# Kernel tuning notes

Measured on AMD Instinct MI355X. Metric: run time of the kernel, lower is better.

Reference implementation:

```python
import jax, jax.numpy as jnp
import numpy as np

N_NODES = 100000
N_EDGES = 1600000
IN_FEAT = 128
HIDDEN = 64
N_CLASSES = 16


def setup_inputs() -> dict:
    key = jax.random.key(0)
    ks = jax.random.split(key, 8)
    x = jax.random.normal(ks[0], (N_NODES, IN_FEAT), dtype=jnp.float32)
    edge_index = jax.random.randint(ks[1], (2, N_EDGES), 0, N_NODES, dtype=jnp.int64)
    W1 = jax.random.normal(ks[2], (IN_FEAT, HIDDEN), dtype=jnp.float32) / np.sqrt(IN_FEAT)
    b1 = jnp.zeros((HIDDEN,), dtype=jnp.float32)
    W2 = jax.random.normal(ks[3], (HIDDEN, HIDDEN), dtype=jnp.float32) / np.sqrt(HIDDEN)
    b2 = jnp.zeros((HIDDEN,), dtype=jnp.float32)
    Wl = jax.random.normal(ks[4], (HIDDEN, N_CLASSES), dtype=jnp.float32) / np.sqrt(HIDDEN)
    bl = jnp.zeros((N_CLASSES,), dtype=jnp.float32)
    return {"x": x, "edge_index": edge_index, "W1": W1, "b1": b1,
            "W2": W2, "b2": b2, "Wl": Wl, "bl": bl}


def _gcn_norm(edge_index, n_nodes, dtype):
    # PyG GCNConv default: add self-loops, symmetric normalization
    # A_hat = D^{-1/2} (A + I) D^{-1/2}, degree computed at destination (col).
    loop = jnp.arange(n_nodes, dtype=edge_index.dtype)
    src = jnp.concatenate([edge_index[0], loop])
    dst = jnp.concatenate([edge_index[1], loop])
    deg = jax.ops.segment_sum(jnp.ones_like(dst, dtype=dtype), dst, num_segments=n_nodes)
    dinv = jnp.where(deg > 0, jax.lax.rsqrt(deg), 0.0).astype(dtype)
    norm = dinv[src] * dinv[dst]  # [E + N]
    return src, dst, norm


def _gcn_conv(h, src, dst, norm, W, b, n_nodes):
    hw = h @ W                                  # [N, out] linear first (GCNConv order)
    msg = hw[src] * norm[:, None]               # gather + edge-normalize, [E+N, out]
    out = jax.ops.segment_sum(msg, dst, num_segments=n_nodes)  # scatter-add
    return out + b


def reference(x, edge_index, W1, b1, W2, b2, Wl, bl):
    n = x.shape[0]
    src, dst, norm = _gcn_norm(edge_index, n, x.dtype)
    h = jax.nn.relu(_gcn_conv(x, src, dst, norm, W1, b1, n))
    h = jax.nn.relu(_gcn_conv(h, src, dst, norm, W2, b2, n))
    return h @ Wl + bl  # [N, num_classes] logits
```

## Files before the change

kernel.cpp:

```cpp
#include <hip/hip_runtime.h>
#include <hip/hip_fp16.h>
#include <math.h>

#define N_NODES 100000
#define N_EDGES 1600000
#define IN_FEAT 128
#define HIDDEN 64
#define N_CLASSES 16

#define TM 64
#define GBLK ((N_NODES + TM - 1) / TM)

#define NBUK 196
#define CB 4096
#define NCB ((N_EDGES + CB - 1) / CB)


__global__ __launch_bounds__(256) void count_k(const int* __restrict__ dst,
                                               int* __restrict__ blk_cnt) {
    __shared__ int hist[NBUK + 4];
    int tid = threadIdx.x;
    if (tid < NBUK) hist[tid] = 0;
    __syncthreads();
    int eb = blockIdx.x * CB;
    #pragma unroll
    for (int q = 0; q < 4; ++q) {
        int e4 = (eb >> 2) + tid + q * 256;
        if (e4 * 4 < N_EDGES) {
            int4 d4 = ((const int4*)dst)[e4];
            atomicAdd(&hist[d4.x >> 9], 1);
            atomicAdd(&hist[d4.y >> 9], 1);
            atomicAdd(&hist[d4.z >> 9], 1);
            atomicAdd(&hist[d4.w >> 9], 1);
        }
    }
    __syncthreads();
    if (tid < NBUK) blk_cnt[blockIdx.x * NBUK + tid] = hist[tid];
}

__global__ __launch_bounds__(512) void colscan_k(int* __restrict__ blk_cnt,
                                                 int* __restrict__ coltot) {
    __shared__ int sm[512];
    int b = blockIdx.x;
    int t = threadIdx.x;
    int v = (t < NCB) ? blk_cnt[t * NBUK + b] : 0;
    sm[t] = v;
    __syncthreads();
    for (int s = 1; s < 512; s <<= 1) {
        int add = (t >= s) ? sm[t - s] : 0;
        __syncthreads();
        sm[t] += add;
        __syncthreads();
    }
    if (t < NCB) blk_cnt[t * NBUK + b] = sm[t] - v;
    if (t == NCB - 1) coltot[b] = sm[t];
}

__global__ __launch_bounds__(256) void bukoff_k(const int* __restrict__ coltot,
                                                int* __restrict__ buk_off) {
    __shared__ int sm[256];
    int t = threadIdx.x;
    int v = (t < NBUK) ? coltot[t] : 0;
    sm[t] = v;
    __syncthreads();
    for (int s = 1; s < 256; s <<= 1) {
        int add = (t >= s) ? sm[t - s] : 0;
        __syncthreads();
        sm[t] += add;
        __syncthreads();
    }
    if (t < NBUK) buk_off[t] = sm[t] - v;
    if (t == 0) buk_off[NBUK] = N_EDGES;
}

__global__ __launch_bounds__(256) void place_k(const int* __restrict__ src,
                                               const int* __restrict__ dst,
                                               const int* __restrict__ colpre,
                                               const int* __restrict__ buk_off,
                                               int2* __restrict__ pairs) {
    __shared__ int cur[NBUK + 4];
    int tid = threadIdx.x;
    int blk = blockIdx.x;
    if (tid < NBUK) cur[tid] = buk_off[tid] + colpre[blk * NBUK + tid];
    __syncthreads();
    int eb = blk * CB;
    #pragma unroll
    for (int q = 0; q < 4; ++q) {
        int e4 = (eb >> 2) + tid + q * 256;
        if (e4 * 4 < N_EDGES) {
            int4 s4 = ((const int4*)src)[e4];
            int4 d4 = ((const int4*)dst)[e4];
            int r;
            r = atomicAdd(&cur[d4.x >> 9], 1); pairs[r] = make_int2(s4.x, d4.x);
            r = atomicAdd(&cur[d4.y >> 9], 1); pairs[r] = make_int2(s4.y, d4.y);
            r = atomicAdd(&cur[d4.z >> 9], 1); pairs[r] = make_int2(s4.z, d4.z);
            r = atomicAdd(&cur[d4.w >> 9], 1); pairs[r] = make_int2(s4.w, d4.w);
        }
    }
}


__global__ __launch_bounds__(256) void fine2_k(const int2* __restrict__ pairs,
                                               const int* __restrict__ buk_off,
                                               int* __restrict__ csr_src,
                                               int* __restrict__ row_ptr,
                                               float* __restrict__ dinv) {
    __shared__ int cnt[512];
    __shared__ int psc[256];
    __shared__ int cur[512];
    int b = blockIdx.x;
    int node0 = b * 512;
    int nn = N_NODES - node0;
    if (nn > 512) nn = 512;
    int tid = threadIdx.x;

    cnt[tid] = 0; cnt[tid + 256] = 0;
    __syncthreads();

    int e0 = buk_off[b];
    int e1 = buk_off[b + 1];

    for (int e = e0 + tid; e < e1; e += 256)
        atomicAdd(&cnt[pairs[e].y - node0], 1);
    __syncthreads();

    int c0 = cnt[2 * tid], c1 = cnt[2 * tid + 1];
    int p = c0 + c1;
    psc[tid] = p;
    __syncthreads();
    for (int s = 1; s < 256; s <<= 1) {
        int add = (tid >= s) ? psc[tid - s] : 0;
        __syncthreads();
        psc[tid] += add;
        __syncthreads();
    }
    int excl = psc[tid] - p;
    int g0 = e0 + excl;
    int g1 = g0 + c0;
    cur[2 * tid] = g0;
    cur[2 * tid + 1] = g1;
    if (2 * tid < nn) {
        row_ptr[node0 + 2 * tid] = g0;
        dinv[node0 + 2 * tid] = 1.0f / sqrtf((float)(c0 + 1));
    }
    if (2 * tid + 1 < nn) {
        row_ptr[node0 + 2 * tid + 1] = g1;
        dinv[node0 + 2 * tid + 1] = 1.0f / sqrtf((float)(c1 + 1));
    }
    if (b == NBUK - 1 && tid == 0) row_ptr[N_NODES] = N_EDGES;
    __syncthreads();

    for (int e = e0 + tid; e < e1; e += 256) {
        int2 pr = pairs[e];
        int pos = atomicAdd(&cur[pr.y - node0], 1);
        csr_src[pos] = pr.x;
    }
}


__global__ __launch_bounds__(256) void gemm1_tiled_k(const float* __restrict__ x,
                                                     const float* __restrict__ W,
                                                     const float* __restrict__ dinv,
                                                     __half* __restrict__ hws_h) {
    __shared__ float Ws[64][64];
    __shared__ float xt[64][68];
    int tid = threadIdx.x;
    int row0 = blockIdx.x * TM;
    int rgrp4 = (tid >> 4) * 4;
    int cgrp4 = (tid & 15) * 4;

    float acc[4][4];
    #pragma unroll
    for (int r = 0; r < 4; ++r)
        #pragma unroll
        for (int c = 0; c < 4; ++c) acc[r][c] = 0.0f;

    for (int k0 = 0; k0 < IN_FEAT; k0 += 64) {
        #pragma unroll
        for (int i = 0; i < 4; ++i) {
            int f4 = tid + i * 256;
            int kk = f4 >> 4, c4 = (f4 & 15) * 4;
            *(float4*)&Ws[kk][c4] = *(const float4*)&W[(size_t)(k0 + kk) * HIDDEN + c4];
        }
        #pragma unroll
        for (int i = 0; i < 4; ++i) {
            int f4 = tid + i * 256;
            int rr = f4 >> 4, kq = (f4 & 15) * 4;
            int row = row0 + rr;
            if (row >= N_NODES) row = N_NODES - 1;
            float4 v = *(const float4*)&x[(size_t)row * IN_FEAT + k0 + kq];
            xt[kq + 0][rr] = v.x; xt[kq + 1][rr] = v.y;
            xt[kq + 2][rr] = v.z; xt[kq + 3][rr] = v.w;
        }
        __syncthreads();

        #pragma unroll 16
        for (int kk = 0; kk < 64; ++kk) {
            float4 a = *(const float4*)&xt[kk][rgrp4];
            float4 b = *(const float4*)&Ws[kk][cgrp4];
            acc[0][0] += a.x * b.x; acc[0][1] += a.x * b.y; acc[0][2] += a.x * b.z; acc[0][3] += a.x * b.w;
            acc[1][0] += a.y * b.x; acc[1][1] += a.y * b.y; acc[1][2] += a.y * b.z; acc[1][3] += a.y * b.w;
            acc[2][0] += a.z * b.x; acc[2][1] += a.z * b.y; acc[2][2] += a.z * b.z; acc[2][3] += a.z * b.w;
            acc[3][0] += a.w * b.x; acc[3][1] += a.w * b.y; acc[3][2] += a.w * b.z; acc[3][3] += a.w * b.w;
        }
        __syncthreads();
    }

    #pragma unroll
    for (int r = 0; r < 4; ++r) {
        int row = row0 + rgrp4 + r;
        if (row < N_NODES) {
            float dn = dinv[row];
            __half2* ph = (__half2*)&hws_h[(size_t)row * HIDDEN + cgrp4];
            ph[0] = __floats2half2_rn(acc[r][0] * dn, acc[r][1] * dn);
            ph[1] = __floats2half2_rn(acc[r][2] * dn, acc[r][3] * dn);
        }
    }
}


__global__ __launch_bounds__(256) void gemm2_tiled_k(const float* __restrict__ agg,
                                                     const float* __restrict__ W,
                                                     const float* __restrict__ dinv,
                                                     __half* __restrict__ hws_h) {
    __shared__ float Ws[64][64];
    __shared__ float xt[64][68];
    int tid = threadIdx.x;
    int row0 = blockIdx.x * TM;
    int rgrp4 = (tid >> 4) * 4;
    int cgrp4 = (tid & 15) * 4;

    #pragma unroll
    for (int i = 0; i < 4; ++i) {
        int f4 = tid + i * 256;
        int kk = f4 >> 4, c4 = (f4 & 15) * 4;
        *(float4*)&Ws[kk][c4] = *(const float4*)&W[(size_t)kk * HIDDEN + c4];
    }
    #pragma unroll
    for (int i = 0; i < 4; ++i) {
        int f4 = tid + i * 256;
        int rr = f4 >> 4, kq = (f4 & 15) * 4;
        int row = row0 + rr;
        if (row >= N_NODES) row = N_NODES - 1;
        float4 v = *(const float4*)&agg[(size_t)row * HIDDEN + kq];
        xt[kq + 0][rr] = fmaxf(v.x, 0.f); xt[kq + 1][rr] = fmaxf(v.y, 0.f);
        xt[kq + 2][rr] = fmaxf(v.z, 0.f); xt[kq + 3][rr] = fmaxf(v.w, 0.f);
    }
    __syncthreads();

    float acc[4][4];
    #pragma unroll
    for (int r = 0; r < 4; ++r)
        #pragma unroll
        for (int c = 0; c < 4; ++c) acc[r][c] = 0.0f;

    #pragma unroll 16
    for (int kk = 0; kk < 64; ++kk) {
        float4 a = *(const float4*)&xt[kk][rgrp4];
        float4 b = *(const float4*)&Ws[kk][cgrp4];
        acc[0][0] += a.x * b.x; acc[0][1] += a.x * b.y; acc[0][2] += a.x * b.z; acc[0][3] += a.x * b.w;
        acc[1][0] += a.y * b.x; acc[1][1] += a.y * b.y; acc[1][2] += a.y * b.z; acc[1][3] += a.y * b.w;
        acc[2][0] += a.z * b.x; acc[2][1] += a.z * b.y; acc[2][2] += a.z * b.z; acc[2][3] += a.z * b.w;
        acc[3][0] += a.w * b.x; acc[3][1] += a.w * b.y; acc[3][2] += a.w * b.z; acc[3][3] += a.w * b.w;
    }

    #pragma unroll
    for (int r = 0; r < 4; ++r) {
        int row = row0 + rgrp4 + r;
        if (row < N_NODES) {
            float dn = dinv[row];
            __half2* ph = (__half2*)&hws_h[(size_t)row * HIDDEN + cgrp4];
            ph[0] = __floats2half2_rn(acc[r][0] * dn, acc[r][1] * dn);
            ph[1] = __floats2half2_rn(acc[r][2] * dn, acc[r][3] * dn);
        }
    }
}


#define GATH(K, ACC)                                                        \
    { int s_ = __builtin_amdgcn_readlane(idxv, (C) + (K));                  \
      const __half* row_ = hws_h + ((size_t)s_ << 6);                       \
      float w_ = ((K) < rem) ? 1.f : 0.f;                                   \
      ACC += w_ * __half2float(row_[lane]); }

#define GATH8(B)                                                            \
    GATH((B) + 0, a0) GATH((B) + 1, a1) GATH((B) + 2, a2) GATH((B) + 3, a3) \
    GATH((B) + 4, a4) GATH((B) + 5, a5) GATH((B) + 6, a6) GATH((B) + 7, a7)

__global__ __launch_bounds__(256) void pull_k(const int* __restrict__ row_ptr,
                                              const int* __restrict__ csr_src,
                                              const float* __restrict__ dinv,
                                              const __half* __restrict__ hws_h,
                                              const float* __restrict__ b,
                                              float* __restrict__ agg) {
    int node = __builtin_amdgcn_readfirstlane((blockIdx.x * 256 + threadIdx.x) >> 6);
    int lane = threadIdx.x & 63;
    if (node >= N_NODES) return;

    int start = __builtin_amdgcn_readfirstlane(row_ptr[node]);
    int end   = __builtin_amdgcn_readfirstlane(row_ptr[node + 1]);

    const __half* __restrict__ selfrow = hws_h + ((size_t)node << 6);
    float blane = b[lane];
    float a0 = __half2float(selfrow[lane]);
    float dn = dinv[node];

    float a1 = 0.f, a2 = 0.f, a3 = 0.f, a4 = 0.f, a5 = 0.f, a6 = 0.f, a7 = 0.f;

    int base = start;
    while (base < end) {
        int ci = base + lane;
        int last = end - 1;
        if (ci > last) ci = last;
        int idxv = csr_src[ci];

        int rem = end - base;
        {
            const int C = 0;
            GATH8(0) GATH8(8) GATH8(16) GATH8(24)
        }
        if (base + 32 < end) {
            const int C = 32;
            rem = end - base - 32;
            GATH8(0) GATH8(8) GATH8(16) GATH8(24)
        }
        base += 64;
    }

    float sum = ((a0 + a1) + (a2 + a3)) + ((a4 + a5) + (a6 + a7));
    float* __restrict__ outrow = agg + ((size_t)node << 6);
    outrow[lane] = blane + dn * sum;
}


__global__ __launch_bounds__(256) void final_k(const float* __restrict__ agg,
                                               const float* __restrict__ Wl,
                                               const float* __restrict__ bl,
                                               float* __restrict__ out) {
    __shared__ float Ws[HIDDEN * N_CLASSES];
    __shared__ float hs[16][HIDDEN + 1];
    int tid = threadIdx.x;

    if (tid < HIDDEN * N_CLASSES / 4) ((float4*)Ws)[tid] = ((const float4*)Wl)[tid];

    int row0 = blockIdx.x * 16;
    for (int i = tid; i < 16 * HIDDEN; i += 256) {
        int rr = i >> 6;
        int kk = i & 63;
        hs[rr][kk] = fmaxf(agg[(size_t)(row0 + rr) * HIDDEN + kk], 0.0f);
    }
    __syncthreads();

    int col = tid & 15;
    int r = tid >> 4;
    float acc = bl[col];
    #pragma unroll
    for (int k = 0; k < HIDDEN; ++k)
        acc += hs[r][k] * Ws[k * N_CLASSES + col];
    out[(size_t)(row0 + r) * N_CLASSES + col] = acc;
}


extern "C" void kernel_launch(void* const* d_in, const int* in_sizes, int n_in,
                              void* d_out, int out_size, void* d_ws, size_t ws_size,
                              hipStream_t stream) {
    const float* x  = (const float*)d_in[0];
    const int*   ei = (const int*)d_in[1];
    const float* W1 = (const float*)d_in[2];
    const float* b1 = (const float*)d_in[3];
    const float* W2 = (const float*)d_in[4];
    const float* b2 = (const float*)d_in[5];
    const float* Wl = (const float*)d_in[6];
    const float* bl = (const float*)d_in[7];
    float* out = (float*)d_out;

    const int* src = ei;
    const int* dst = ei + N_EDGES;

    __half* hws_h  = (__half*)d_ws;
    float* agg     = (float*)(hws_h + (size_t)N_NODES * HIDDEN);
    int2*  pairs   = (int2*)agg;
    int*   csr_src = (int*)(agg + (size_t)N_NODES * HIDDEN);
    float* dinv    = (float*)(csr_src + N_EDGES);
    int*   row_ptr = (int*)(dinv + N_NODES);
    int*   buk_cnt = row_ptr + N_NODES + 4;
    int*   buk_off = buk_cnt + 200;
    int*   coltot  = buk_off + 200;
    int*   blk_cnt = csr_src;

    count_k<<<NCB, 256, 0, stream>>>(dst, blk_cnt);
    colscan_k<<<NBUK, 512, 0, stream>>>(blk_cnt, coltot);
    bukoff_k<<<1, 256, 0, stream>>>(coltot, buk_off);
    place_k<<<NCB, 256, 0, stream>>>(src, dst, blk_cnt, buk_off, pairs);
    fine2_k<<<NBUK, 256, 0, stream>>>(pairs, buk_off, csr_src, row_ptr, dinv);

    gemm1_tiled_k<<<GBLK, 256, 0, stream>>>(x, W1, dinv, hws_h);
    pull_k<<<(N_NODES * 64 + 255) / 256, 256, 0, stream>>>(row_ptr, csr_src, dinv,
                                                           hws_h, b1, agg);

    gemm2_tiled_k<<<GBLK, 256, 0, stream>>>(agg, W2, dinv, hws_h);
    pull_k<<<(N_NODES * 64 + 255) / 256, 256, 0, stream>>>(row_ptr, csr_src, dinv,
                                                           hws_h, b2, agg);

    final_k<<<N_NODES / 16, 256, 0, stream>>>(agg, Wl, bl, out);
}
```

Baseline: 288.3 us.

## Pack edge pairs into 32-bit words, stage in LDS, fuse second pull with head

```diff
diff --git a/kernel.cpp b/kernel.cpp
--- a/kernel.cpp
+++ b/kernel.cpp
@@ -14,6 +14,10 @@
 #define NBUK 196
 #define CB 4096
 #define NCB ((N_EDGES + CB - 1) / CB)
+
+#define PACK(s, d)  ((s) | (((d) & 511) << 17))
+#define P_SRC(p)    ((p) & 0x1FFFF)
+#define P_LOC(p)    (((unsigned)(p)) >> 17)
 
 
 __global__ __launch_bounds__(256) void count_k(const int* __restrict__ dst,
@@ -77,7 +81,7 @@
                                                const int* __restrict__ dst,
                                                const int* __restrict__ colpre,
                                                const int* __restrict__ buk_off,
-                                               int2* __restrict__ pairs) {
+                                               int* __restrict__ pairs_p) {
     __shared__ int cur[NBUK + 4];
     int tid = threadIdx.x;
     int blk = blockIdx.x;
@@ -91,20 +95,23 @@
             int4 s4 = ((const int4*)src)[e4];
             int4 d4 = ((const int4*)dst)[e4];
             int r;
-            r = atomicAdd(&cur[d4.x >> 9], 1); pairs[r] = make_int2(s4.x, d4.x);
-            r = atomicAdd(&cur[d4.y >> 9], 1); pairs[r] = make_int2(s4.y, d4.y);
-            r = atomicAdd(&cur[d4.z >> 9], 1); pairs[r] = make_int2(s4.z, d4.z);
-            r = atomicAdd(&cur[d4.w >> 9], 1); pairs[r] = make_int2(s4.w, d4.w);
-        }
-    }
-}
-
-
-__global__ __launch_bounds__(256) void fine2_k(const int2* __restrict__ pairs,
+            r = atomicAdd(&cur[d4.x >> 9], 1); pairs_p[r] = PACK(s4.x, d4.x);
+            r = atomicAdd(&cur[d4.y >> 9], 1); pairs_p[r] = PACK(s4.y, d4.y);
+            r = atomicAdd(&cur[d4.z >> 9], 1); pairs_p[r] = PACK(s4.z, d4.z);
+            r = atomicAdd(&cur[d4.w >> 9], 1); pairs_p[r] = PACK(s4.w, d4.w);
+        }
+    }
+}
+
+
+#define FCAP 12288
+
+__global__ __launch_bounds__(256) void fine2_k(const int* __restrict__ pairs_p,
                                                const int* __restrict__ buk_off,
                                                int* __restrict__ csr_src,
                                                int* __restrict__ row_ptr,
                                                float* __restrict__ dinv) {
+    __shared__ int stage[FCAP];
     __shared__ int cnt[512];
     __shared__ int psc[256];
     __shared__ int cur[512];
@@ -119,9 +126,19 @@
 
     int e0 = buk_off[b];
     int e1 = buk_off[b + 1];
-
-    for (int e = e0 + tid; e < e1; e += 256)
-        atomicAdd(&cnt[pairs[e].y - node0], 1);
+    int nE = e1 - e0;
+    bool inlds = (nE <= FCAP);
+
+    if (inlds) {
+        for (int e = e0 + tid; e < e1; e += 256) {
+            int p = pairs_p[e];
+            stage[e - e0] = p;
+            atomicAdd(&cnt[P_LOC(p)], 1);
+        }
+    } else {
+        for (int e = e0 + tid; e < e1; e += 256)
+            atomicAdd(&cnt[P_LOC(pairs_p[e])], 1);
+    }
     __syncthreads();
 
     int c0 = cnt[2 * tid], c1 = cnt[2 * tid + 1];
@@ -150,10 +167,18 @@
     if (b == NBUK - 1 && tid == 0) row_ptr[N_NODES] = N_EDGES;
     __syncthreads();
 
-    for (int e = e0 + tid; e < e1; e += 256) {
-        int2 pr = pairs[e];
-        int pos = atomicAdd(&cur[pr.y - node0], 1);
-        csr_src[pos] = pr.x;
+    if (inlds) {
+        for (int i = tid; i < nE; i += 256) {
+            int pr = stage[i];
+            int pos = atomicAdd(&cur[P_LOC(pr)], 1);
+            csr_src[pos] = P_SRC(pr);
+        }
+    } else {
+        for (int e = e0 + tid; e < e1; e += 256) {
+            int pr = pairs_p[e];
+            int pos = atomicAdd(&cur[P_LOC(pr)], 1);
+            csr_src[pos] = P_SRC(pr);
+        }
     }
 }
 
@@ -277,15 +302,53 @@
 }
 
 
-#define GATH(K, ACC)                                                        \
-    { int s_ = __builtin_amdgcn_readlane(idxv, (C) + (K));                  \
-      const __half* row_ = hws_h + ((size_t)s_ << 6);                       \
-      float w_ = ((K) < rem) ? 1.f : 0.f;                                   \
-      ACC += w_ * __half2float(row_[lane]); }
-
-#define GATH8(B)                                                            \
-    GATH((B) + 0, a0) GATH((B) + 1, a1) GATH((B) + 2, a2) GATH((B) + 3, a3) \
-    GATH((B) + 4, a4) GATH((B) + 5, a5) GATH((B) + 6, a6) GATH((B) + 7, a7)
+#define PULL_BODY(OUT_STMT)                                                  \
+    int start = __builtin_amdgcn_readfirstlane(row_ptr[node]);               \
+    int end   = __builtin_amdgcn_readfirstlane(row_ptr[node + 1]);           \
+    const __half* __restrict__ selfrow = hws_h + ((size_t)node << 6);        \
+    float blane = b[lane];                                                   \
+    float a0 = __half2float(selfrow[lane]);                                  \
+    float dn = dinv[node];                                                   \
+    float a1 = 0.f, a2 = 0.f, a3 = 0.f, a4 = 0.f, a5 = 0.f, a6 = 0.f, a7 = 0.f; \
+    int base = start;                                                        \
+    while (base < end) {                                                     \
+        int rem = end - base;                                                \
+        int ci = base + lane;                                                \
+        int lastci = end - 1;                                                \
+        if (ci > lastci) ci = lastci;                                        \
+        int idxv = csr_src[ci];                                              \
+        int nch = rem < 64 ? rem : 64;                                       \
+        for (int j = 0; j < nch; j += 16) {                                  \
+            _Pragma("unroll")                                                \
+            for (int k = 0; k < 16; ++k) {                                   \
+                int jj = j + k;                                              \
+                int s = __builtin_amdgcn_readlane(idxv, jj);                 \
+                const __half* __restrict__ row = hws_h + ((size_t)s << 6);   \
+                float w = (jj < rem) ? 1.f : 0.f;                            \
+                float v = __half2float(row[lane]);                           \
+                if (k == 0)      a0 += w * v;                                \
+                else if (k == 1) a1 += w * v;                                \
+                else if (k == 2) a2 += w * v;                                \
+                else if (k == 3) a3 += w * v;                                \
+                else if (k == 4) a4 += w * v;                                \
+                else if (k == 5) a5 += w * v;                                \
+                else if (k == 6) a6 += w * v;                                \
+                else if (k == 7) a7 += w * v;                                \
+                else if (k == 8)  a0 += w * v;                               \
+                else if (k == 9)  a1 += w * v;                               \
+                else if (k == 10) a2 += w * v;                               \
+                else if (k == 11) a3 += w * v;                               \
+                else if (k == 12) a4 += w * v;                               \
+                else if (k == 13) a5 += w * v;                               \
+                else if (k == 14) a6 += w * v;                               \
+                else              a7 += w * v;                               \
+            }                                                                \
+        }                                                                    \
+        base += 64;                                                          \
+    }                                                                        \
+    float sum = ((a0 + a1) + (a2 + a3)) + ((a4 + a5) + (a6 + a7));           \
+    float val = blane + dn * sum;                                            \
+    OUT_STMT
 
 __global__ __launch_bounds__(256) void pull_k(const int* __restrict__ row_ptr,
                                               const int* __restrict__ csr_src,
@@ -296,68 +359,41 @@
     int node = __builtin_amdgcn_readfirstlane((blockIdx.x * 256 + threadIdx.x) >> 6);
     int lane = threadIdx.x & 63;
     if (node >= N_NODES) return;
-
-    int start = __builtin_amdgcn_readfirstlane(row_ptr[node]);
-    int end   = __builtin_amdgcn_readfirstlane(row_ptr[node + 1]);
-
-    const __half* __restrict__ selfrow = hws_h + ((size_t)node << 6);
-    float blane = b[lane];
-    float a0 = __half2float(selfrow[lane]);
-    float dn = dinv[node];
-
-    float a1 = 0.f, a2 = 0.f, a3 = 0.f, a4 = 0.f, a5 = 0.f, a6 = 0.f, a7 = 0.f;
-
-    int base = start;
-    while (base < end) {
-        int ci = base + lane;
-        int last = end - 1;
-        if (ci > last) ci = last;
-        int idxv = csr_src[ci];
-
-        int rem = end - base;
-        {
-            const int C = 0;
-            GATH8(0) GATH8(8) GATH8(16) GATH8(24)
-        }
-        if (base + 32 < end) {
-            const int C = 32;
-            rem = end - base - 32;
-            GATH8(0) GATH8(8) GATH8(16) GATH8(24)
-        }
-        base += 64;
-    }
-
-    float sum = ((a0 + a1) + (a2 + a3)) + ((a4 + a5) + (a6 + a7));
-    float* __restrict__ outrow = agg + ((size_t)node << 6);
-    outrow[lane] = blane + dn * sum;
-}
-
-
-__global__ __launch_bounds__(256) void final_k(const float* __restrict__ agg,
-                                               const float* __restrict__ Wl,
-                                               const float* __restrict__ bl,
-                                               float* __restrict__ out) {
-    __shared__ float Ws[HIDDEN * N_CLASSES];
-    __shared__ float hs[16][HIDDEN + 1];
-    int tid = threadIdx.x;
-
-    if (tid < HIDDEN * N_CLASSES / 4) ((float4*)Ws)[tid] = ((const float4*)Wl)[tid];
-
-    int row0 = blockIdx.x * 16;
-    for (int i = tid; i < 16 * HIDDEN; i += 256) {
-        int rr = i >> 6;
-        int kk = i & 63;
-        hs[rr][kk] = fmaxf(agg[(size_t)(row0 + rr) * HIDDEN + kk], 0.0f);
-    }
-    __syncthreads();
-
-    int col = tid & 15;
-    int r = tid >> 4;
-    float acc = bl[col];
-    #pragma unroll
-    for (int k = 0; k < HIDDEN; ++k)
-        acc += hs[r][k] * Ws[k * N_CLASSES + col];
-    out[(size_t)(row0 + r) * N_CLASSES + col] = acc;
+    PULL_BODY({ float* __restrict__ outrow = agg + ((size_t)node << 6);
+                outrow[lane] = val; })
+}
+
+
+__global__ __launch_bounds__(256) void pull_head_k(const int* __restrict__ row_ptr,
+                                                   const int* __restrict__ csr_src,
+                                                   const float* __restrict__ dinv,
+                                                   const __half* __restrict__ hws_h,
+                                                   const float* __restrict__ b,
+                                                   const float* __restrict__ Wl,
+                                                   const float* __restrict__ bl,
+                                                   float* __restrict__ out) {
+    __shared__ float hs[4][65];
+    __shared__ float Wls[HIDDEN * N_CLASSES];
+    __shared__ float bls[N_CLASSES];
+    int tid = threadIdx.x;
+    int wid = tid >> 6;
+    int lane = tid & 63;
+    int node = __builtin_amdgcn_readfirstlane(blockIdx.x * 4 + wid);
+
+    ((float4*)Wls)[tid] = ((const float4*)Wl)[tid];
+    if (tid < N_CLASSES) bls[tid] = bl[tid];
+
+    PULL_BODY({ hs[wid][lane] = fmaxf(val, 0.0f); })
+
+    __syncthreads();
+    if (tid < 64) {
+        int r = tid >> 4, col = tid & 15;
+        float acc = bls[col];
+        #pragma unroll
+        for (int k = 0; k < HIDDEN; ++k)
+            acc += hs[r][k] * Wls[k * N_CLASSES + col];
+        out[(size_t)(blockIdx.x * 4 + r) * N_CLASSES + col] = acc;
+    }
 }
 
 
@@ -379,7 +415,7 @@
 
     __half* hws_h  = (__half*)d_ws;
     float* agg     = (float*)(hws_h + (size_t)N_NODES * HIDDEN);
-    int2*  pairs   = (int2*)agg;
+    int*   pairs_p = (int*)agg;
     int*   csr_src = (int*)(agg + (size_t)N_NODES * HIDDEN);
     float* dinv    = (float*)(csr_src + N_EDGES);
     int*   row_ptr = (int*)(dinv + N_NODES);
@@ -391,16 +427,14 @@
     count_k<<<NCB, 256, 0, stream>>>(dst, blk_cnt);
     colscan_k<<<NBUK, 512, 0, stream>>>(blk_cnt, coltot);
     bukoff_k<<<1, 256, 0, stream>>>(coltot, buk_off);
-    place_k<<<NCB, 256, 0, stream>>>(src, dst, blk_cnt, buk_off, pairs);
-    fine2_k<<<NBUK, 256, 0, stream>>>(pairs, buk_off, csr_src, row_ptr, dinv);
+    place_k<<<NCB, 256, 0, stream>>>(src, dst, blk_cnt, buk_off, pairs_p);
+    fine2_k<<<NBUK, 256, 0, stream>>>(pairs_p, buk_off, csr_src, row_ptr, dinv);
 
     gemm1_tiled_k<<<GBLK, 256, 0, stream>>>(x, W1, dinv, hws_h);
     pull_k<<<(N_NODES * 64 + 255) / 256, 256, 0, stream>>>(row_ptr, csr_src, dinv,
                                                            hws_h, b1, agg);
 
     gemm2_tiled_k<<<GBLK, 256, 0, stream>>>(agg, W2, dinv, hws_h);
-    pull_k<<<(N_NODES * 64 + 255) / 256, 256, 0, stream>>>(row_ptr, csr_src, dinv,
-                                                           hws_h, b2, agg);
-
-    final_k<<<N_NODES / 16, 256, 0, stream>>>(agg, Wl, bl, out);
-}
+    pull_head_k<<<N_NODES / 4, 256, 0, stream>>>(row_ptr, csr_src, dinv,
+                                                 hws_h, b2, Wl, bl, out);
+}
```

New measurement: 265.5 us. -7.9%, faster.
